# Performance work log

Hardware: AMD Instinct MI355X
Metric: run time of the kernel (lower is better)

The kernel has to match this reference:

```python
import jax, jax.numpy as jnp
import numpy as np

EMBED_DIM = 768
NUM_HEADS = 12
HEAD_DIM = EMBED_DIM // NUM_HEADS  # 64
SEGMENT_LENGTHS = (2048, 4096, 8192)
DILATION_RATES = (1, 2, 4)
LN_EPS = 1e-5


def setup_inputs() -> dict:
    key = jax.random.key(0)
    ks = jax.random.split(key, 8)
    B, N, E = 2, 8192, EMBED_DIM
    std = 1.0 / np.sqrt(E)
    return {
        "query": jax.random.normal(ks[0], (B, N, E), jnp.float32),
        "key": jax.random.normal(ks[1], (B, N, E), jnp.float32),
        "value": jax.random.normal(ks[2], (B, N, E), jnp.float32),
        "Wqkv": jax.random.normal(ks[3], (3 * E, E), jnp.float32) * std,
        "bqkv": jnp.zeros((3 * E,), jnp.float32),
        "Wo": jax.random.normal(ks[4], (E, E), jnp.float32) * std,
        "bo": jnp.zeros((E,), jnp.float32),
        "ln_w": jnp.ones((E,), jnp.float32),
        "ln_b": jnp.zeros((E,), jnp.float32),
        "is_causal": 0,
    }


def _dilated_attention(q, k, v, is_causal):
    # q, k, v: (b, n, h, d). Heads are partitioned into len(SEGMENT_LENGTHS) groups.
    b, n, h, d = q.shape
    ng = len(SEGMENT_LENGTHS)
    g = h // ng  # heads per group
    scale = 1.0 / np.sqrt(d)
    outs = []
    for i, (s, r) in enumerate(zip(SEGMENT_LENGTHS, DILATION_RATES)):
        off = i % r
        hs = slice(i * g, (i + 1) * g)
        m = n // s          # number of segments
        t = (s - off + r - 1) // r  # dilated tokens per segment
        # (b, m, s, g, d) -> dilated subsample -> (b, m, t, g, d)
        qi = q[:, :, hs].reshape(b, m, s, g, d)[:, :, off::r] * scale
        ki = k[:, :, hs].reshape(b, m, s, g, d)[:, :, off::r]
        vi = v[:, :, hs].reshape(b, m, s, g, d)[:, :, off::r]
        # attention within each segment over the dilated tokens
        scores = jnp.einsum("bmqhd,bmkhd->bmhqk", qi, ki)  # (b,m,g,t,t)
        if is_causal:
            mask = jnp.tril(jnp.ones((t, t), bool))
            scores = jnp.where(mask, scores, jnp.finfo(scores.dtype).min)
        attn = jax.nn.softmax(scores, axis=-1)
        xi = jnp.einsum("bmhqk,bmkhd->bmqhd", attn, vi)  # (b,m,t,g,d)
        # scatter back into full segment positions (zeros elsewhere)
        full = jnp.zeros((b, m, s, g, d), xi.dtype).at[:, :, off::r].set(xi)
        outs.append(full.reshape(b, n, g, d))
    return jnp.concatenate(outs, axis=2)  # (b, n, h, d)


def reference(query, key, value, Wqkv, bqkv, Wo, bo, ln_w, ln_b, is_causal):
    b, n, e = query.shape
    h, d = NUM_HEADS, HEAD_DIM
    q = (query @ Wqkv[:e].T + bqkv[:e]).reshape(b, n, h, d)
    k = (key @ Wqkv[e:2 * e].T + bqkv[e:2 * e]).reshape(b, n, h, d)
    v = (value @ Wqkv[2 * e:].T + bqkv[2 * e:]).reshape(b, n, h, d)
    x = _dilated_attention(q, k, v, is_causal).reshape(b, n, e)
    # LayerNorm
    mu = jnp.mean(x, axis=-1, keepdims=True)
    var = jnp.mean(jnp.square(x - mu), axis=-1, keepdims=True)
    x = (x - mu) * jax.lax.rsqrt(var + LN_EPS) * ln_w + ln_b
    return x @ Wo.T + bo
```

## Files before the change

kernel.cpp:

```cpp
#include <hip/hip_runtime.h>
#include <stdint.h>
#include <stddef.h>

typedef __bf16 bf16;
typedef __attribute__((ext_vector_type(4))) float f32x4;
typedef __attribute__((ext_vector_type(16))) float f32x16;
typedef __attribute__((ext_vector_type(8))) bf16 bf16x8;
typedef __attribute__((ext_vector_type(4))) bf16 bf16x4;

#define INST_STRIDE (2048 * 64)

static __device__ __forceinline__ f32x4 mfma16(bf16x8 a, bf16x8 b, f32x4 c) {
  return __builtin_amdgcn_mfma_f32_16x16x32_bf16(a, b, c, 0, 0, 0);
}
static __device__ __forceinline__ f32x16 mfma32(bf16x8 a, bf16x8 b, f32x16 c) {
  return __builtin_amdgcn_mfma_f32_32x32x16_bf16(a, b, c, 0, 0, 0);
}
static __device__ __forceinline__ void gload16(const void* g, void* l) {
  __builtin_amdgcn_global_load_lds(
      (const __attribute__((address_space(1))) void*)g,
      (__attribute__((address_space(3))) void*)l, 16, 0, 0);
}
static __device__ __forceinline__ float exp2_fast(float x) {
  float r;
  asm("v_exp_f32 %0, %1" : "=v"(r) : "v"(x));
  return r;
}

__global__ void convert_w(const float* __restrict__ Wqkv, const float* __restrict__ Wo,
                          bf16* __restrict__ wq, bf16* __restrict__ wo) {
  int idx = blockIdx.x * 256 + threadIdx.x;
  const int NQ = 3 * 768 * 768 / 4;
  const float4* src;
  bf16* dst;
  int i;
  if (idx < NQ) { src = (const float4*)Wqkv; dst = wq; i = idx; }
  else          { src = (const float4*)Wo;   dst = wo; i = idx - NQ; }
  float4 v = src[i];
  bf16x4 o = { (bf16)v.x, (bf16)v.y, (bf16)v.z, (bf16)v.w };
  *(bf16x4*)(dst + (size_t)i * 4) = o;
}

__launch_bounds__(512, 2)
__global__ void qkv_gemm(const float* __restrict__ Xq, const float* __restrict__ Xk,
                         const float* __restrict__ Xv, const bf16* __restrict__ Wb,
                         const float* __restrict__ bqkv, bf16* __restrict__ qg,
                         bf16* __restrict__ kg, bf16* __restrict__ vtg) {
  __shared__ __align__(16) bf16 lA[128 * 64];
  __shared__ __align__(16) bf16 lB[256 * 64];
  const int z = blockIdx.z;
  const float* __restrict__ X = (z == 0) ? Xq : ((z == 1) ? Xk : Xv);
  const int bx = blockIdx.x;
  int g, mt;
  if (bx < 128)      { g = 0; mt = bx; }
  else if (bx < 192) { g = 1; mt = bx - 128; }
  else               { g = 2; mt = bx - 192; }
  const int gshift = 13 - g;
  const int gpbm = (8192 >> g) - 1;
  const int ibase = (g == 2) ? 24 : (g << 4);
  const int nseg = 4 >> g;

  const int tid = threadIdx.x;
  const int lane = tid & 63, w = tid >> 6;
  const int wr = w >> 2, wc = w & 3;
  const int l15 = lane & 15, lg = lane >> 4;

  auto maprow = [&](int G) -> size_t {
    int bb = G >> gshift;
    int loc = G & gpbm;
    int seg = loc >> 11, tq = loc & 2047;
    int token = (seg << (11 + g)) + g + (tq << g);
    return (size_t)(bb * 8192 + token);
  };

  const int c8 = tid & 7;
  size_t arow[2];
  int rr[2];
#pragma unroll
  for (int i = 0; i < 2; ++i) {
    rr[i] = i * 64 + (tid >> 3);
    arow[i] = maprow(mt * 128 + rr[i]);
  }

  f32x4 acc[4][4];
#pragma unroll
  for (int i = 0; i < 4; ++i)
#pragma unroll
    for (int j = 0; j < 4; ++j) acc[i][j] = (f32x4){0.f, 0.f, 0.f, 0.f};

  for (int t = 0; t < 12; ++t) {
    const int k0 = t * 64;
#pragma unroll
    for (int j = 0; j < 4; ++j) {
      int region = w * 4 + j;
      int row = region * 8 + (lane >> 3);
      int cb = lane & 7;
      const bf16* src = Wb + (size_t)(z * 768 + g * 256 + row) * 768 + k0 + ((cb ^ (row & 7)) << 3);
      gload16(src, (char*)lB + region * 1024);
    }
#pragma unroll
    for (int i = 0; i < 2; ++i) {
      const float* src = X + arow[i] * 768 + k0 + c8 * 8;
      float4 v0 = ((const float4*)src)[0];
      float4 v1 = ((const float4*)src)[1];
      bf16x8 o = { (bf16)v0.x, (bf16)v0.y, (bf16)v0.z, (bf16)v0.w,
                   (bf16)v1.x, (bf16)v1.y, (bf16)v1.z, (bf16)v1.w };
      *(bf16x8*)((char*)lA + rr[i] * 128 + ((c8 ^ (rr[i] & 7)) << 4)) = o;
    }
    __syncthreads();
#pragma unroll
    for (int ks = 0; ks < 2; ++ks) {
      bf16x8 af[4], bfr[4];
#pragma unroll
      for (int i = 0; i < 4; ++i) {
        int row = wr * 64 + i * 16 + l15;
        af[i] = *(const bf16x8*)((const char*)lA + row * 128 + (((ks * 4 + lg) ^ (row & 7)) << 4));
        int col = wc * 64 + i * 16 + l15;
        bfr[i] = *(const bf16x8*)((const char*)lB + col * 128 + (((ks * 4 + lg) ^ (col & 7)) << 4));
      }
      __builtin_amdgcn_s_setprio(1);
#pragma unroll
      for (int i = 0; i < 4; ++i)
#pragma unroll
        for (int j = 0; j < 4; ++j) acc[i][j] = mfma16(af[i], bfr[j], acc[i][j]);
      __builtin_amdgcn_s_setprio(0);
    }
    __syncthreads();
  }
#pragma unroll
  for (int j = 0; j < 4; ++j) {
    int col = wc * 64 + j * 16 + l15;
    float bias = bqkv[z * 768 + g * 256 + col];
    int hg = col >> 6, d = col & 63;
    int ho = ibase + hg * nseg;
#pragma unroll
    for (int i = 0; i < 4; ++i) {
      int G0 = mt * 128 + wr * 64 + i * 16 + (lg << 2);
      if (z == 2) {
        int bb = G0 >> gshift;
        int loc = G0 & gpbm;
        int seg = loc >> 11, tq = loc & 2047;
        size_t io = (size_t)(bb * 28 + ho + seg) * INST_STRIDE;
        int tsw = (tq & ~63) | ((((tq >> 3) & 7) ^ (d & 7)) << 3) | (tq & 7);
        bf16x4 pk = { (bf16)(acc[i][j][0] + bias), (bf16)(acc[i][j][1] + bias),
                      (bf16)(acc[i][j][2] + bias), (bf16)(acc[i][j][3] + bias) };
        *(bf16x4*)(vtg + io + (size_t)d * 2048 + tsw) = pk;
      } else {
#pragma unroll
        for (int reg = 0; reg < 4; ++reg) {
          int G = G0 + reg;
          int bb = G >> gshift;
          int loc = G & gpbm;
          int seg = loc >> 11, tq = loc & 2047;
          size_t io = (size_t)(bb * 28 + ho + seg) * INST_STRIDE;
          float v = acc[i][j][reg] + bias;
          if (z == 0) {
            qg[io + tq * 64 + d] = (bf16)(v * 0.180336880f);
          } else {
            int dsw = (d & 7) | (((d >> 3) ^ (tq & 7)) << 3);
            kg[io + tq * 64 + dsw] = (bf16)v;
          }
        }
      }
    }
  }
}

#define CVTPK(lo_, hi_, out_) \
  asm("v_cvt_pk_bf16_f32 %0, %1, %2" : "=v"(out_) : "v"(lo_), "v"(hi_))

#define MAKE_PA(sv, kb2, dst)                                              \
  do {                                                                     \
    float p0 = exp2_fast(sv[kb2 * 8 + 0]);                                 \
    float p1 = exp2_fast(sv[kb2 * 8 + 1]);                                 \
    float p2 = exp2_fast(sv[kb2 * 8 + 2]);                                 \
    float p3 = exp2_fast(sv[kb2 * 8 + 3]);                                 \
    float p4 = exp2_fast(sv[kb2 * 8 + 4]);                                 \
    float p5 = exp2_fast(sv[kb2 * 8 + 5]);                                 \
    float p6 = exp2_fast(sv[kb2 * 8 + 6]);                                 \
    float p7 = exp2_fast(sv[kb2 * 8 + 7]);                                 \
    rs += (p0 + p1) + (p2 + p3) + ((p4 + p5) + (p6 + p7));                 \
    uint32_t a0, a1, a2, a3;                                               \
    CVTPK(p0, p1, a0); CVTPK(p2, p3, a1);                                  \
    CVTPK(p4, p5, a2); CVTPK(p6, p7, a3);                                  \
    asm("v_permlane32_swap_b32 %0, %1" : "+v"(a0), "+v"(a2));              \
    asm("v_permlane32_swap_b32 %0, %1" : "+v"(a1), "+v"(a3));              \
    union { uint32_t u[4]; bf16x8 v; } pk_;                                \
    pk_.u[0] = a0; pk_.u[1] = a1; pk_.u[2] = a2; pk_.u[3] = a3;            \
    dst = pk_.v;                                                           \
  } while (0)

__launch_bounds__(256, 2)
__global__ void attn(const bf16* __restrict__ qg, const bf16* __restrict__ kg,
                     const bf16* __restrict__ vtg, bf16* __restrict__ og,
                     const int* __restrict__ causal_p) {
  __shared__ __align__(16) bf16 lK[2][64 * 64];
  __shared__ __align__(16) bf16 lV[2][64 * 64];
  __shared__ float lSc[4][32];
  const int L = blockIdx.x + (blockIdx.y << 4);
  const int inst = (L & 7) * 7 + ((L >> 3) >> 4);
  const int qt = (L >> 3) & 15;
  const int tid = threadIdx.x, lane = tid & 63, w = tid >> 6;
  const int l31 = lane & 31, hi = lane >> 5;
  const int causal = causal_p[0];
  const size_t ib = (size_t)inst * INST_STRIDE;
  const int qbase = qt * 128 + w * 32;

  bf16x8 qf[4];
#pragma unroll
  for (int dt4 = 0; dt4 < 4; ++dt4)
    qf[dt4] = *(const bf16x8*)(qg + ib + (size_t)(qbase + l31) * 64 + dt4 * 16 + hi * 8);

  int off0[4], off1[4];
#pragma unroll
  for (int c = 0; c < 4; ++c) {
    off0[c] = l31 * 128 + (((c * 2 + hi) ^ (l31 & 7)) << 4);
    off1[c] = (32 + l31) * 128 + (((c * 2 + hi) ^ (l31 & 7)) << 4);
  }

  f32x16 oacc0 = {0}, oacc1 = {0};
  float l = 0.f;

#define STAGE_AT(buf, kt_)                                                       \
  do {                                                                           \
    _Pragma("unroll") for (int j = 0; j < 2; ++j) {                              \
      int region = w * 2 + j;                                                    \
      int r = region * 8 + (lane >> 3);                                          \
      int cb = lane & 7;                                                         \
      gload16(kg + ib + (size_t)((kt_) + r) * 64 + cb * 8,                       \
              (char*)lK[buf] + region * 1024);                                   \
      gload16(vtg + ib + (size_t)r * 2048 + (kt_) + cb * 8,                      \
              (char*)lV[buf] + region * 1024);                                   \
    }                                                                            \
  } while (0)

  STAGE_AT(0, 0);
  __syncthreads();
  int cur = 0;
  for (int kt = 0; kt < 2048; kt += 64) {
    if (kt + 64 < 2048) STAGE_AT(cur ^ 1, kt + 64);
    const char* K = (const char*)lK[cur];
    const char* V = (const char*)lV[cur];
    f32x16 st0 = {0}, st1 = {0};
    __builtin_amdgcn_s_setprio(1);
#pragma unroll
    for (int dt4 = 0; dt4 < 4; ++dt4) {
      bf16x8 kf0 = *(const bf16x8*)(K + off0[dt4]);
      bf16x8 kf1 = *(const bf16x8*)(K + off1[dt4]);
      st0 = mfma32(kf0, qf[dt4], st0);
      st1 = mfma32(kf1, qf[dt4], st1);
    }
    __builtin_amdgcn_s_setprio(0);
    if (causal) {
      int q = qbase + l31;
#pragma unroll
      for (int r = 0; r < 16; ++r) {
        int kl = (r & 3) + 8 * (r >> 2) + 4 * hi;
        if (kt + kl > q) st0[r] = -1e30f;
        if (kt + 32 + kl > q) st1[r] = -1e30f;
      }
    }
    float rs = 0.f;
    bf16x8 pa0, pa1, pa2, pa3;
    MAKE_PA(st0, 0, pa0);
    MAKE_PA(st0, 1, pa1);
    MAKE_PA(st1, 0, pa2);
    MAKE_PA(st1, 1, pa3);
    rs += __shfl_xor(rs, 32);
    l += rs;
    __builtin_amdgcn_s_setprio(1);
#pragma unroll
    for (int kb = 0; kb < 4; ++kb) {
      bf16x8 pak = (kb == 0) ? pa0 : (kb == 1) ? pa1 : (kb == 2) ? pa2 : pa3;
      bf16x8 vf0 = *(const bf16x8*)(V + off0[kb]);
      bf16x8 vf1 = *(const bf16x8*)(V + off1[kb]);
      oacc0 = mfma32(pak, vf0, oacc0);
      oacc1 = mfma32(pak, vf1, oacc1);
    }
    __builtin_amdgcn_s_setprio(0);
    __syncthreads();
    cur ^= 1;
  }
  if (!hi) lSc[w][l31] = 1.f / l;
  asm volatile("s_waitcnt lgkmcnt(0)" ::: "memory");
  __builtin_amdgcn_sched_barrier(0);
#pragma unroll
  for (int r = 0; r < 16; ++r) {
    int ql = (r & 3) + 8 * (r >> 2) + 4 * hi;
    float linv = lSc[w][ql];
    int q = qbase + ql;
    og[ib + (size_t)q * 64 + l31] = (bf16)(oacc0[r] * linv);
    og[ib + (size_t)q * 64 + 32 + l31] = (bf16)(oacc1[r] * linv);
  }
}

__global__ void ln_gather(const bf16* __restrict__ og, const float* __restrict__ lnw,
                          const float* __restrict__ lnb, bf16* __restrict__ xnorm) {
  const int tok = blockIdx.x * 4 + (threadIdx.x >> 6);
  const int lane = threadIdx.x & 63;
  const int bb = tok >> 13, n = tok & 8191;
  float vals[12];
#pragma unroll
  for (int h = 0; h < 12; ++h) {
    const int grp = h >> 2, hg = h & 3;
    const int sl = 11 + grp;
    int pos = n & ((1 << sl) - 1), seg = n >> sl;
    int rel = pos - grp;
    float v = 0.f;
    if (rel >= 0 && (rel & ((1 << grp) - 1)) == 0) {
      int tq = rel >> grp;
      int base = (grp == 2) ? 24 : (grp << 4);
      size_t inst = (size_t)(bb * 28 + base + hg * (4 >> grp) + seg);
      v = (float)og[inst * INST_STRIDE + (size_t)tq * 64 + lane];
    }
    vals[h] = v;
  }
  float sum = 0.f, sq = 0.f;
#pragma unroll
  for (int h = 0; h < 12; ++h) { sum += vals[h]; sq += vals[h] * vals[h]; }
#pragma unroll
  for (int mm = 32; mm; mm >>= 1) { sum += __shfl_xor(sum, mm); sq += __shfl_xor(sq, mm); }
  const float mu = sum * (1.f / 768.f);
  const float var = sq * (1.f / 768.f) - mu * mu;
  const float rstd = rsqrtf(var + 1e-5f);
  const int tok7 = tok & 7;
#pragma unroll
  for (int h = 0; h < 12; ++h) {
    int e = h * 64 + lane;
    float xn = (vals[h] - mu) * rstd * lnw[e] + lnb[e];
    int esw = h * 64 + ((((lane >> 3) ^ tok7) << 3) | (lane & 7));
    xnorm[(size_t)tok * 768 + esw] = (bf16)xn;
  }
}

__launch_bounds__(512, 2)
__global__ void out_gemm(const bf16* __restrict__ xn, const bf16* __restrict__ wo,
                         const float* __restrict__ bo, float* __restrict__ out) {
  __shared__ __align__(16) bf16 lA[128 * 64];
  __shared__ __align__(16) bf16 lB[256 * 64];
  const int mt = blockIdx.x, nt = blockIdx.y;
  const int tid = threadIdx.x, lane = tid & 63, w = tid >> 6;
  const int wr = w >> 2, wc = w & 3;
  const int l15 = lane & 15, lg = lane >> 4;
  f32x4 acc[4][4];
#pragma unroll
  for (int i = 0; i < 4; ++i)
#pragma unroll
    for (int j = 0; j < 4; ++j) acc[i][j] = (f32x4){0.f, 0.f, 0.f, 0.f};

  for (int k0 = 0; k0 < 768; k0 += 64) {
#pragma unroll
    for (int j = 0; j < 2; ++j) {
      int region = w * 2 + j;
      int r = region * 8 + (lane >> 3);
      int cb = lane & 7;
      gload16(xn + (size_t)(mt * 128 + r) * 768 + k0 + cb * 8, (char*)lA + region * 1024);
    }
#pragma unroll
    for (int j = 0; j < 4; ++j) {
      int region = w * 4 + j;
      int r = region * 8 + (lane >> 3);
      int cb = lane & 7;
      gload16(wo + (size_t)(nt * 256 + r) * 768 + k0 + ((cb ^ (r & 7)) << 3), (char*)lB + region * 1024);
    }
    __syncthreads();
#pragma unroll
    for (int ks = 0; ks < 2; ++ks) {
      bf16x8 af[4], bfr[4];
#pragma unroll
      for (int i = 0; i < 4; ++i) {
        int row = wr * 64 + i * 16 + l15;
        af[i] = *(const bf16x8*)((const char*)lA + row * 128 + (((ks * 4 + lg) ^ (row & 7)) << 4));
        int col = wc * 64 + i * 16 + l15;
        bfr[i] = *(const bf16x8*)((const char*)lB + col * 128 + (((ks * 4 + lg) ^ (col & 7)) << 4));
      }
      __builtin_amdgcn_s_setprio(1);
#pragma unroll
      for (int i = 0; i < 4; ++i)
#pragma unroll
        for (int j = 0; j < 4; ++j) acc[i][j] = mfma16(af[i], bfr[j], acc[i][j]);
      __builtin_amdgcn_s_setprio(0);
    }
    __syncthreads();
  }
#pragma unroll
  for (int j = 0; j < 4; ++j) {
    int col = nt * 256 + wc * 64 + j * 16 + l15;
    float bias = bo[col];
#pragma unroll
    for (int i = 0; i < 4; ++i) {
      int row0 = mt * 128 + wr * 64 + i * 16 + (lg << 2);
#pragma unroll
      for (int reg = 0; reg < 4; ++reg)
        out[(size_t)(row0 + reg) * 768 + col] = acc[i][j][reg] + bias;
    }
  }
}

extern "C" void kernel_launch(void* const* d_in, const int* in_sizes, int n_in,
                              void* d_out, int out_size, void* d_ws, size_t ws_size,
                              hipStream_t stream) {
  (void)in_sizes; (void)n_in; (void)out_size; (void)ws_size;
  const float* query = (const float*)d_in[0];
  const float* key_  = (const float*)d_in[1];
  const float* value = (const float*)d_in[2];
  const float* Wqkv  = (const float*)d_in[3];
  const float* bqkv  = (const float*)d_in[4];
  const float* Wo    = (const float*)d_in[5];
  const float* bo    = (const float*)d_in[6];
  const float* lnw   = (const float*)d_in[7];
  const float* lnb   = (const float*)d_in[8];
  const int* flag    = (const int*)d_in[9];
  float* out = (float*)d_out;

  char* ws = (char*)d_ws;
  size_t off = 0;
  auto alloc = [&](size_t bytes) -> char* {
    char* p = ws + off;
    off += (bytes + 255) & ~(size_t)255;
    return p;
  };
  bf16* wq_bf  = (bf16*)alloc((size_t)3 * 768 * 768 * 2);
  bf16* wo_bf  = (bf16*)alloc((size_t)768 * 768 * 2);
  bf16* qg     = (bf16*)alloc((size_t)56 * INST_STRIDE * 2);
  bf16* kg     = (bf16*)alloc((size_t)56 * INST_STRIDE * 2);
  bf16* vtg    = (bf16*)alloc((size_t)56 * INST_STRIDE * 2);
  bf16* og     = (bf16*)alloc((size_t)56 * INST_STRIDE * 2);
  bf16* xnorm  = (bf16*)alloc((size_t)16384 * 768 * 2);

  convert_w<<<dim3(2304), dim3(256), 0, stream>>>(Wqkv, Wo, wq_bf, wo_bf);
  qkv_gemm<<<dim3(224, 1, 3), dim3(512), 0, stream>>>(query, key_, value, wq_bf, bqkv, qg, kg, vtg);
  attn<<<dim3(16, 56), dim3(256), 0, stream>>>(qg, kg, vtg, og, flag);
  ln_gather<<<dim3(4096), dim3(256), 0, stream>>>(og, lnw, lnb, xnorm);
  out_gemm<<<dim3(128, 3), dim3(512), 0, stream>>>(xnorm, wo_bf, bo, out);
}
```

Measured before the change: 208.9 us.

## Prefetch next A tile into registers and use explicit waitcnt barriers in QKV GEMM

The QKV projection loop now issues the fp32 activation loads for the next K-step before the current step's compute, holding them in registers. It also precomputes the weight-tile source pointers. The __syncthreads calls are replaced with explicit s_waitcnt plus s_barrier, so the prefetched A loads can stay in flight across the barrier. The intent is to hide global load latency behind the MFMA work, at the cost of extra registers and more fragile hand-placed wait counts.

```diff
diff --git a/kernel.cpp b/kernel.cpp
--- a/kernel.cpp
+++ b/kernel.cpp
@@ -81,6 +81,14 @@
     rr[i] = i * 64 + (tid >> 3);
     arow[i] = maprow(mt * 128 + rr[i]);
   }
+  const bf16* bsrc[4];
+#pragma unroll
+  for (int j = 0; j < 4; ++j) {
+    int region = w * 4 + j;
+    int row = region * 8 + (lane >> 3);
+    int cb = lane & 7;
+    bsrc[j] = Wb + (size_t)(z * 768 + g * 256 + row) * 768 + ((cb ^ (row & 7)) << 3);
+  }
 
   f32x4 acc[4][4];
 #pragma unroll
@@ -88,26 +96,38 @@
 #pragma unroll
     for (int j = 0; j < 4; ++j) acc[i][j] = (f32x4){0.f, 0.f, 0.f, 0.f};
 
+  float4 apf[2][2];
+  auto ISSUE_A = [&](int t) {
+#pragma unroll
+    for (int i = 0; i < 2; ++i) {
+      const float* src = X + arow[i] * 768 + t * 64 + c8 * 8;
+      apf[i][0] = ((const float4*)src)[0];
+      apf[i][1] = ((const float4*)src)[1];
+    }
+  };
+
+  ISSUE_A(0);
   for (int t = 0; t < 12; ++t) {
-    const int k0 = t * 64;
-#pragma unroll
-    for (int j = 0; j < 4; ++j) {
-      int region = w * 4 + j;
-      int row = region * 8 + (lane >> 3);
-      int cb = lane & 7;
-      const bf16* src = Wb + (size_t)(z * 768 + g * 256 + row) * 768 + k0 + ((cb ^ (row & 7)) << 3);
-      gload16(src, (char*)lB + region * 1024);
-    }
+    asm volatile("s_waitcnt vmcnt(0)" ::: "memory");
+    __builtin_amdgcn_sched_barrier(0);
 #pragma unroll
     for (int i = 0; i < 2; ++i) {
-      const float* src = X + arow[i] * 768 + k0 + c8 * 8;
-      float4 v0 = ((const float4*)src)[0];
-      float4 v1 = ((const float4*)src)[1];
+      float4 v0 = apf[i][0], v1 = apf[i][1];
       bf16x8 o = { (bf16)v0.x, (bf16)v0.y, (bf16)v0.z, (bf16)v0.w,
                    (bf16)v1.x, (bf16)v1.y, (bf16)v1.z, (bf16)v1.w };
       *(bf16x8*)((char*)lA + rr[i] * 128 + ((c8 ^ (rr[i] & 7)) << 4)) = o;
     }
-    __syncthreads();
+#pragma unroll
+    for (int j = 0; j < 4; ++j)
+      gload16(bsrc[j] + t * 64, (char*)lB + (w * 4 + j) * 1024);
+    if (t < 11) {
+      ISSUE_A(t + 1);
+      asm volatile("s_waitcnt vmcnt(4) lgkmcnt(0)" ::: "memory");
+    } else {
+      asm volatile("s_waitcnt vmcnt(0) lgkmcnt(0)" ::: "memory");
+    }
+    __builtin_amdgcn_sched_barrier(0);
+    __builtin_amdgcn_s_barrier();
 #pragma unroll
     for (int ks = 0; ks < 2; ++ks) {
       bf16x8 af[4], bfr[4];
@@ -125,7 +145,8 @@
         for (int j = 0; j < 4; ++j) acc[i][j] = mfma16(af[i], bfr[j], acc[i][j]);
       __builtin_amdgcn_s_setprio(0);
     }
-    __syncthreads();
+    __builtin_amdgcn_sched_barrier(0);
+    __builtin_amdgcn_s_barrier();
   }
 #pragma unroll
   for (int j = 0; j < 4; ++j) {
```

After: 219.4 us. 5.0% more time.
